# Kernel optimization log

Measured on AMD Instinct MI355X. Metric: run time of the kernel, lower is better.

Reference implementation:

```python
import jax, jax.numpy as jnp
import numpy as np

K = 5  # Chebyshev order


def laplacian(w):
    # normalized Laplacian: I - D^{-1/2} W D^{-1/2}
    d = jnp.sum(w, axis=1)
    d_re = 1.0 / jnp.sqrt(d + 1e-5)
    return jnp.eye(w.shape[0], dtype=w.dtype) - d_re[:, None] * w * d_re[None, :]


def cheb_terms(x, lap, k):
    # x: [B,N,C], lap: [N,N] -> [B,k,N,C]
    # Faithful to torch code: T0 = ones, then (x, lap@x) recurrence for k>2.
    t0 = jnp.ones_like(x)
    if k == 1:
        return t0[:, None]
    t1 = jnp.matmul(lap, x)
    if k == 2:
        return jnp.stack([t0, t1], axis=1)
    terms = [t0, x, t1]
    tkm1, tk = x, t1
    for _ in range(3, k):
        tkm1, tk = tk, 2.0 * jnp.matmul(lap, tk) - tkm1
        terms.append(tk)
    return jnp.stack(terms, axis=1)


def graph_conv(x, lap, w, k):
    # torch: cp.permute(0,2,3,1).flatten(2) @ w, i.e. flat index = c*k + t
    t = cheb_terms(x, lap, k)                       # [B,k,N,C]
    C = x.shape[-1]
    O = w.shape[-1]
    return jnp.einsum('bknc,cko->bno', t, w.reshape(C, k, O))


def setup_inputs() -> dict:
    key = jax.random.key(0)
    ks = jax.random.split(key, 9)
    B, N, Cin, H = 8192, 32, 60, 128
    return {
        'x': jax.random.normal(ks[0], (B, N, Cin), dtype=jnp.float32),
        'adj': jax.random.normal(ks[1], (N, N), dtype=jnp.float32) * 0.1,
        'adj_bias': jax.random.normal(ks[2], (1,), dtype=jnp.float32) * 0.1 + 0.2,
        'w1': jax.random.normal(ks[3], (K * Cin, H), dtype=jnp.float32) * 0.05,
        'b1': jax.random.normal(ks[4], (1, 1, H), dtype=jnp.float32) * 0.05,
        'w2': jax.random.normal(ks[5], (K * H, H), dtype=jnp.float32) * 0.05,
        'b2': jax.random.normal(ks[6], (1, 1, H), dtype=jnp.float32) * 0.05,
        'fc_w': jax.random.normal(ks[7], (2, N * H), dtype=jnp.float32) * 0.02,
        'fc_b': jax.random.normal(ks[8], (2,), dtype=jnp.float32) * 0.02,
    }


def reference(x, adj, adj_bias, w1, b1, w2, b2, fc_w, fc_b):
    # DGCNN.forward (eval mode: dropout = identity)
    a = jax.nn.relu(adj + adj_bias)
    lap = laplacian(a)
    h = graph_conv(x, lap, w1, K)
    h = jax.nn.relu(h + b1)      # B1ReLU
    h = graph_conv(h, lap, w2, K)
    h = jax.nn.relu(h + b2)
    h = h.reshape(h.shape[0], -1)  # [B, N*H]
    return h @ fc_w.T + fc_b
```

## Files before the change

### kernel.cpp

```cpp
#include <hip/hip_runtime.h>

typedef unsigned short u16;
typedef unsigned int u32;
typedef short bf16x8 __attribute__((ext_vector_type(8)));
typedef float f32x4 __attribute__((ext_vector_type(4)));

#define MFMA16(a, b, c) __builtin_amdgcn_mfma_f32_16x16x32_bf16((a), (b), (c), 0, 0, 0)

__device__ __forceinline__ u16 f2bf(float f) {
  u32 u = __builtin_bit_cast(u32, f);
  u += 0x7FFFu + ((u >> 16) & 1u);
  return (u16)(u >> 16);
}
__device__ __forceinline__ u32 pk2bf(float a, float b) {
#if __has_builtin(__builtin_amdgcn_cvt_pk_bf16_f32)
  auto v = __builtin_amdgcn_cvt_pk_bf16_f32(a, b);
  return __builtin_bit_cast(u32, v);
#else
  return (u32)f2bf(a) | ((u32)f2bf(b) << 16);
#endif
}

#define WS_MGF   0
#define WS_WT1F  8192
#define WS_WT2F  73728
#define WS_B1    204800
#define WS_B2    205312

__global__ void prep_kernel(const float* __restrict__ adj,
                            const float* __restrict__ adj_bias,
                            const float* __restrict__ w1,
                            const float* __restrict__ b1,
                            const float* __restrict__ w2,
                            const float* __restrict__ b2,
                            char* __restrict__ ws) {
  const int tid = threadIdx.x;
  if (blockIdx.x == 0) {
    __shared__ float sa[1024], Ls[1024], L2s[1024], L3s[1024], sdre[32];
    float bias = adj_bias[0];
    for (int i = tid; i < 1024; i += 256) sa[i] = fmaxf(adj[i] + bias, 0.0f);
    __syncthreads();
    if (tid < 32) {
      float s = 0.0f;
      for (int c = 0; c < 32; ++c) s += sa[tid * 32 + c];
      sdre[tid] = 1.0f / sqrtf(s + 1e-5f);
    }
    __syncthreads();
    for (int i = tid; i < 1024; i += 256) {
      int n = i >> 5, c = i & 31;
      Ls[i] = (n == c ? 1.0f : 0.0f) - sdre[n] * sa[i] * sdre[c];
    }
    __syncthreads();
    for (int i = tid; i < 1024; i += 256) {
      int r = i >> 5, c = i & 31;
      float s = 0.0f;
      for (int m = 0; m < 32; ++m) s += Ls[r * 32 + m] * Ls[m * 32 + c];
      L2s[i] = s;
    }
    __syncthreads();
    for (int i = tid; i < 1024; i += 256) {
      int r = i >> 5, c = i & 31;
      float s = 0.0f;
      for (int m = 0; m < 32; ++m) s += L2s[r * 32 + m] * Ls[m * 32 + c];
      L3s[i] = s;
    }
    __syncthreads();
    u16* MGf = (u16*)(ws + WS_MGF);
    for (int i = tid; i < 4096; i += 256) {
      int jt = i >> 9, lane = (i >> 3) & 63, j = i & 7;
      int col = jt * 16 + (lane & 15);
      int k = ((lane >> 4) << 3) + j;
      int kk = col >> 5, np = col & 31;
      float v;
      if (kk == 0)      v = (np == k) ? 1.0f : 0.0f;
      else if (kk == 1) v = Ls[np * 32 + k];
      else if (kk == 2) v = 2.0f * L2s[np * 32 + k] - (np == k ? 1.0f : 0.0f);
      else              v = 4.0f * L3s[np * 32 + k] - 3.0f * Ls[np * 32 + k];
      MGf[i] = f2bf(v);
    }
    float* B1 = (float*)(ws + WS_B1);
    float* B2 = (float*)(ws + WS_B2);
    if (tid < 128) {
      float s = b1[tid];
      for (int c = 0; c < 60; ++c) s += w1[(c * 5) * 128 + tid];
      B1[tid] = s;
    } else {
      int o = tid - 128;
      float s = b2[o];
      for (int c = 0; c < 128; ++c) s += w2[(c * 5) * 128 + o];
      B2[o] = s;
    }
  } else {
    u16* WT1F = (u16*)(ws + WS_WT1F);
    u16* WT2F = (u16*)(ws + WS_WT2F);
    int g = (blockIdx.x - 1) * 256 + tid;
    for (int i = g; i < 32768; i += 16 * 256) {
      int ot = i >> 12, ks = (i >> 9) & 7, lane = (i >> 3) & 63, j = i & 7;
      int o = ot * 16 + (lane & 15);
      int kc = ks * 32 + ((lane >> 4) << 3) + j;
      int k = kc >> 6, c = kc & 63;
      WT1F[i] = (c < 60) ? f2bf(w1[(c * 5 + k + 1) * 128 + o]) : (u16)0;
    }
    for (int i = g; i < 65536; i += 16 * 256) {
      int mt = i >> 13, h = (i >> 12) & 1, ks = (i >> 9) & 7;
      int lane = (i >> 3) & 63, j = i & 7;
      int kc = ((ks >> 1) << 7) + ((ks & 1) << 5) + (h << 6) + (((lane >> 4)) << 3) + j;
      int k = kc >> 7, c = kc & 127;
      int o = (mt << 4) + (lane & 15);
      WT2F[i] = f2bf(w2[(c * 5 + k + 1) * 128 + o]);
    }
  }
}

__global__ __launch_bounds__(256, 3) void dgcnn_kernel(
    const float* __restrict__ x,
    const char* __restrict__ ws,
    const float* __restrict__ fc_w,
    const float* __restrict__ fc_b,
    float* __restrict__ out) {
  __shared__ __align__(16) char arena[27136];
  __shared__ float red[8];
  u16* Xt = (u16*)arena;
  u16* Ht = (u16*)arena;
  u16* Y  = (u16*)(arena + 10240);

  const u16* MGf  = (const u16*)(ws + WS_MGF);
  const u16* WT1F = (const u16*)(ws + WS_WT1F);
  const u16* WT2F = (const u16*)(ws + WS_WT2F);
  const float* bias1 = (const float*)(ws + WS_B1);
  const float* bias2 = (const float*)(ws + WS_B2);

  const int tid = threadIdx.x;
  const int w = tid >> 6, lane = tid & 63;
  const int l15 = lane & 15, q = lane >> 4;
  const int b = blockIdx.x;
  const f32x4 z4 = {0.0f, 0.0f, 0.0f, 0.0f};

  bf16x8 mB0 = *(const bf16x8*)(MGf + ((2 * w + 0) * 64 + lane) * 8);
  bf16x8 mB1 = *(const bf16x8*)(MGf + ((2 * w + 1) * 64 + lane) * 8);
  bf16x8 wf1[16];
#pragma unroll
  for (int ot = 0; ot < 2; ++ot)
#pragma unroll
    for (int ks = 0; ks < 8; ++ks)
      wf1[ot * 8 + ks] = *(const bf16x8*)(WT1F + (((2 * w + ot) * 8 + ks) * 64 + lane) * 8);

  for (int i = tid; i < 160; i += 256) Xt[(60 + (i / 40)) * 40 + (i % 40)] = 0;
  const float* xb = x + (size_t)b * 1920;
  for (int i = tid; i < 1920; i += 256) {
    int n = i / 60, c = i - n * 60;
    Xt[c * 40 + n] = f2bf(xb[i]);
  }
  __syncthreads();

  {
    f32x4 acc[4][2];
#pragma unroll
    for (int mt = 0; mt < 4; ++mt) {
      bf16x8 aX = *(const bf16x8*)&Xt[(mt * 16 + l15) * 40 + q * 8];
      acc[mt][0] = MFMA16(aX, mB0, z4);
      acc[mt][1] = MFMA16(aX, mB1, z4);
    }
#pragma unroll
    for (int mt = 0; mt < 4; ++mt)
#pragma unroll
      for (int jt = 0; jt < 2; ++jt) {
        int np = jt * 16 + l15;
        uint2 vv;
        vv.x = pk2bf(acc[mt][jt][0], acc[mt][jt][1]);
        vv.y = pk2bf(acc[mt][jt][2], acc[mt][jt][3]);
        *(uint2*)&Y[np * 264 + w * 64 + mt * 16 + q * 4] = vv;
      }
  }
  __syncthreads();

  {
    f32x4 acc[2][2] = {{z4, z4}, {z4, z4}};
#pragma unroll
    for (int ks = 0; ks < 8; ++ks) {
      bf16x8 a0 = *(const bf16x8*)&Y[(l15) * 264 + ks * 32 + q * 8];
      bf16x8 a1 = *(const bf16x8*)&Y[(16 + l15) * 264 + ks * 32 + q * 8];
      acc[0][0] = MFMA16(a0, wf1[ks], acc[0][0]);
      acc[0][1] = MFMA16(a0, wf1[8 + ks], acc[0][1]);
      acc[1][0] = MFMA16(a1, wf1[ks], acc[1][0]);
      acc[1][1] = MFMA16(a1, wf1[8 + ks], acc[1][1]);
    }
#pragma unroll
    for (int ot = 0; ot < 2; ++ot) {
      int o = (2 * w + ot) * 16 + l15;
      float bv = bias1[o];
#pragma unroll
      for (int mt = 0; mt < 2; ++mt) {
        uint2 vv;
        vv.x = pk2bf(fmaxf(acc[mt][ot][0] + bv, 0.0f), fmaxf(acc[mt][ot][1] + bv, 0.0f));
        vv.y = pk2bf(fmaxf(acc[mt][ot][2] + bv, 0.0f), fmaxf(acc[mt][ot][3] + bv, 0.0f));
        *(uint2*)&Ht[o * 40 + mt * 16 + q * 4] = vv;
      }
    }
  }
  __syncthreads();

  f32x4 acc2[2][2] = {{z4, z4}, {z4, z4}};
#pragma unroll
  for (int h = 0; h < 2; ++h) {
    bf16x8 wf2[16];
#pragma unroll
    for (int ot = 0; ot < 2; ++ot)
#pragma unroll
      for (int ks = 0; ks < 8; ++ks)
        wf2[ot * 8 + ks] =
            *(const bf16x8*)(WT2F + ((((2 * w + ot) * 2 + h) * 8 + ks) * 64 + lane) * 8);

    {
      f32x4 acc[4][2];
#pragma unroll
      for (int mtl = 0; mtl < 4; ++mtl) {
        int mt = 4 * h + mtl;
        bf16x8 aH = *(const bf16x8*)&Ht[(mt * 16 + l15) * 40 + q * 8];
        acc[mtl][0] = MFMA16(aH, mB0, z4);
        acc[mtl][1] = MFMA16(aH, mB1, z4);
      }
#pragma unroll
      for (int mtl = 0; mtl < 4; ++mtl)
#pragma unroll
        for (int jt = 0; jt < 2; ++jt) {
          int np = jt * 16 + l15;
          uint2 vv;
          vv.x = pk2bf(acc[mtl][jt][0], acc[mtl][jt][1]);
          vv.y = pk2bf(acc[mtl][jt][2], acc[mtl][jt][3]);
          *(uint2*)&Y[np * 264 + w * 64 + mtl * 16 + q * 4] = vv;
        }
    }
    __syncthreads();
#pragma unroll
    for (int ks = 0; ks < 8; ++ks) {
      bf16x8 by0 = *(const bf16x8*)&Y[(l15) * 264 + ks * 32 + q * 8];
      bf16x8 by1 = *(const bf16x8*)&Y[(16 + l15) * 264 + ks * 32 + q * 8];
      acc2[0][0] = MFMA16(wf2[ks], by0, acc2[0][0]);
      acc2[0][1] = MFMA16(wf2[ks], by1, acc2[0][1]);
      acc2[1][0] = MFMA16(wf2[8 + ks], by0, acc2[1][0]);
      acc2[1][1] = MFMA16(wf2[8 + ks], by1, acc2[1][1]);
    }
    __syncthreads();
  }

  float p0 = 0.0f, p1 = 0.0f;
#pragma unroll
  for (int ot = 0; ot < 2; ++ot) {
    int ob = (2 * w + ot) * 16 + q * 4;
    float4 bv = *(const float4*)&bias2[ob];
#pragma unroll
    for (int nt = 0; nt < 2; ++nt) {
      int n = nt * 16 + l15;
      float h0 = fmaxf(acc2[ot][nt][0] + bv.x, 0.0f);
      float h1 = fmaxf(acc2[ot][nt][1] + bv.y, 0.0f);
      float h2 = fmaxf(acc2[ot][nt][2] + bv.z, 0.0f);
      float h3 = fmaxf(acc2[ot][nt][3] + bv.w, 0.0f);
      float4 w0 = *(const float4*)&fc_w[n * 128 + ob];
      float4 w1v = *(const float4*)&fc_w[4096 + n * 128 + ob];
      p0 = fmaf(h0, w0.x, fmaf(h1, w0.y, fmaf(h2, w0.z, fmaf(h3, w0.w, p0))));
      p1 = fmaf(h0, w1v.x, fmaf(h1, w1v.y, fmaf(h2, w1v.z, fmaf(h3, w1v.w, p1))));
    }
  }
#pragma unroll
  for (int off = 32; off >= 1; off >>= 1) {
    p0 += __shfl_xor(p0, off);
    p1 += __shfl_xor(p1, off);
  }
  if (lane == 0) {
    red[w * 2 + 0] = p0;
    red[w * 2 + 1] = p1;
  }
  __syncthreads();
  if (tid < 2) {
    out[b * 2 + tid] = red[tid] + red[2 + tid] + red[4 + tid] + red[6 + tid] + fc_b[tid];
  }
}

extern "C" void kernel_launch(void* const* d_in, const int* in_sizes, int n_in,
                              void* d_out, int out_size, void* d_ws, size_t ws_size,
                              hipStream_t stream) {
  const float* x        = (const float*)d_in[0];
  const float* adj      = (const float*)d_in[1];
  const float* adj_bias = (const float*)d_in[2];
  const float* w1       = (const float*)d_in[3];
  const float* b1       = (const float*)d_in[4];
  const float* w2       = (const float*)d_in[5];
  const float* b2       = (const float*)d_in[6];
  const float* fc_w     = (const float*)d_in[7];
  const float* fc_b     = (const float*)d_in[8];
  float* out = (float*)d_out;
  char* ws   = (char*)d_ws;

  prep_kernel<<<17, 256, 0, stream>>>(adj, adj_bias, w1, b1, w2, b2, ws);
  dgcnn_kernel<<<8192, 256, 0, stream>>>(x, ws, fc_w, fc_b, out);
}
```

Before: 206.5 us.

## Process two batch samples per block to reuse weight fragments

Each block now handles two graph samples with duplicated LDS buffers and accumulators, halving the grid to 4096 blocks. Weight fragments for both layers (and the Laplacian fragments) are loaded once and applied to both samples, cutting the global weight traffic and fixed per-block overhead per sample. The first-layer weights are now loaded inside the k-loop instead of held in registers. The H tile stride is also shrunk from 40 to 36. The cost is about double the LDS per block (~52KB) and more accumulator registers, which may lower occupancy.

```diff
diff --git a/kernel.cpp b/kernel.cpp
--- a/kernel.cpp
+++ b/kernel.cpp
@@ -118,11 +118,14 @@
     const float* __restrict__ fc_w,
     const float* __restrict__ fc_b,
     float* __restrict__ out) {
-  __shared__ __align__(16) char arena[27136];
-  __shared__ float red[8];
-  u16* Xt = (u16*)arena;
-  u16* Ht = (u16*)arena;
-  u16* Y  = (u16*)(arena + 10240);
+  __shared__ __align__(16) char arena[52224];
+  __shared__ float red[16];
+  u16* XtA = (u16*)arena;
+  u16* XtB = (u16*)(arena + 5120);
+  u16* HtA = (u16*)arena;
+  u16* HtB = (u16*)(arena + 9216);
+  u16* YA  = (u16*)(arena + 18432);
+  u16* YB  = (u16*)(arena + 35328);
 
   const u16* MGf  = (const u16*)(ws + WS_MGF);
   const u16* WT1F = (const u16*)(ws + WS_WT1F);
@@ -133,57 +136,73 @@
   const int tid = threadIdx.x;
   const int w = tid >> 6, lane = tid & 63;
   const int l15 = lane & 15, q = lane >> 4;
-  const int b = blockIdx.x;
+  const int b0 = blockIdx.x * 2;
   const f32x4 z4 = {0.0f, 0.0f, 0.0f, 0.0f};
 
   bf16x8 mB0 = *(const bf16x8*)(MGf + ((2 * w + 0) * 64 + lane) * 8);
   bf16x8 mB1 = *(const bf16x8*)(MGf + ((2 * w + 1) * 64 + lane) * 8);
-  bf16x8 wf1[16];
-#pragma unroll
-  for (int ot = 0; ot < 2; ++ot)
-#pragma unroll
-    for (int ks = 0; ks < 8; ++ks)
-      wf1[ot * 8 + ks] = *(const bf16x8*)(WT1F + (((2 * w + ot) * 8 + ks) * 64 + lane) * 8);
-
-  for (int i = tid; i < 160; i += 256) Xt[(60 + (i / 40)) * 40 + (i % 40)] = 0;
-  const float* xb = x + (size_t)b * 1920;
+
+  for (int i = tid; i < 160; i += 256) {
+    int r = 60 + i / 40, c = i % 40;
+    XtA[r * 40 + c] = 0;
+    XtB[r * 40 + c] = 0;
+  }
+  const float* xb = x + (size_t)b0 * 1920;
   for (int i = tid; i < 1920; i += 256) {
     int n = i / 60, c = i - n * 60;
-    Xt[c * 40 + n] = f2bf(xb[i]);
+    XtA[c * 40 + n] = f2bf(xb[i]);
+    XtB[c * 40 + n] = f2bf(xb[1920 + i]);
   }
   __syncthreads();
 
   {
-    f32x4 acc[4][2];
+    f32x4 accA[4][2], accB[4][2];
 #pragma unroll
     for (int mt = 0; mt < 4; ++mt) {
-      bf16x8 aX = *(const bf16x8*)&Xt[(mt * 16 + l15) * 40 + q * 8];
-      acc[mt][0] = MFMA16(aX, mB0, z4);
-      acc[mt][1] = MFMA16(aX, mB1, z4);
+      bf16x8 aXA = *(const bf16x8*)&XtA[(mt * 16 + l15) * 40 + q * 8];
+      bf16x8 aXB = *(const bf16x8*)&XtB[(mt * 16 + l15) * 40 + q * 8];
+      accA[mt][0] = MFMA16(aXA, mB0, z4);
+      accA[mt][1] = MFMA16(aXA, mB1, z4);
+      accB[mt][0] = MFMA16(aXB, mB0, z4);
+      accB[mt][1] = MFMA16(aXB, mB1, z4);
     }
 #pragma unroll
     for (int mt = 0; mt < 4; ++mt)
 #pragma unroll
       for (int jt = 0; jt < 2; ++jt) {
         int np = jt * 16 + l15;
-        uint2 vv;
-        vv.x = pk2bf(acc[mt][jt][0], acc[mt][jt][1]);
-        vv.y = pk2bf(acc[mt][jt][2], acc[mt][jt][3]);
-        *(uint2*)&Y[np * 264 + w * 64 + mt * 16 + q * 4] = vv;
+        int off = np * 264 + w * 64 + mt * 16 + q * 4;
+        uint2 vA, vB;
+        vA.x = pk2bf(accA[mt][jt][0], accA[mt][jt][1]);
+        vA.y = pk2bf(accA[mt][jt][2], accA[mt][jt][3]);
+        vB.x = pk2bf(accB[mt][jt][0], accB[mt][jt][1]);
+        vB.y = pk2bf(accB[mt][jt][2], accB[mt][jt][3]);
+        *(uint2*)&YA[off] = vA;
+        *(uint2*)&YB[off] = vB;
       }
   }
   __syncthreads();
 
   {
-    f32x4 acc[2][2] = {{z4, z4}, {z4, z4}};
+    f32x4 accA[2][2] = {{z4, z4}, {z4, z4}};
+    f32x4 accB[2][2] = {{z4, z4}, {z4, z4}};
 #pragma unroll
     for (int ks = 0; ks < 8; ++ks) {
-      bf16x8 a0 = *(const bf16x8*)&Y[(l15) * 264 + ks * 32 + q * 8];
-      bf16x8 a1 = *(const bf16x8*)&Y[(16 + l15) * 264 + ks * 32 + q * 8];
-      acc[0][0] = MFMA16(a0, wf1[ks], acc[0][0]);
-      acc[0][1] = MFMA16(a0, wf1[8 + ks], acc[0][1]);
-      acc[1][0] = MFMA16(a1, wf1[ks], acc[1][0]);
-      acc[1][1] = MFMA16(a1, wf1[8 + ks], acc[1][1]);
+      bf16x8 wfa = *(const bf16x8*)(WT1F + (((2 * w + 0) * 8 + ks) * 64 + lane) * 8);
+      bf16x8 wfb = *(const bf16x8*)(WT1F + (((2 * w + 1) * 8 + ks) * 64 + lane) * 8);
+      int offY = ks * 32 + q * 8;
+      bf16x8 a0A = *(const bf16x8*)&YA[(l15) * 264 + offY];
+      bf16x8 a1A = *(const bf16x8*)&YA[(16 + l15) * 264 + offY];
+      bf16x8 a0B = *(const bf16x8*)&YB[(l15) * 264 + offY];
+      bf16x8 a1B = *(const bf16x8*)&YB[(16 + l15) * 264 + offY];
+      accA[0][0] = MFMA16(a0A, wfa, accA[0][0]);
+      accA[0][1] = MFMA16(a0A, wfb, accA[0][1]);
+      accA[1][0] = MFMA16(a1A, wfa, accA[1][0]);
+      accA[1][1] = MFMA16(a1A, wfb, accA[1][1]);
+      accB[0][0] = MFMA16(a0B, wfa, accB[0][0]);
+      accB[0][1] = MFMA16(a0B, wfb, accB[0][1]);
+      accB[1][0] = MFMA16(a1B, wfa, accB[1][0]);
+      accB[1][1] = MFMA16(a1B, wfb, accB[1][1]);
     }
 #pragma unroll
     for (int ot = 0; ot < 2; ++ot) {
@@ -191,16 +210,21 @@
       float bv = bias1[o];
 #pragma unroll
       for (int mt = 0; mt < 2; ++mt) {
-        uint2 vv;
-        vv.x = pk2bf(fmaxf(acc[mt][ot][0] + bv, 0.0f), fmaxf(acc[mt][ot][1] + bv, 0.0f));
-        vv.y = pk2bf(fmaxf(acc[mt][ot][2] + bv, 0.0f), fmaxf(acc[mt][ot][3] + bv, 0.0f));
-        *(uint2*)&Ht[o * 40 + mt * 16 + q * 4] = vv;
+        int off = o * 36 + mt * 16 + q * 4;
+        uint2 vA, vB;
+        vA.x = pk2bf(fmaxf(accA[mt][ot][0] + bv, 0.0f), fmaxf(accA[mt][ot][1] + bv, 0.0f));
+        vA.y = pk2bf(fmaxf(accA[mt][ot][2] + bv, 0.0f), fmaxf(accA[mt][ot][3] + bv, 0.0f));
+        vB.x = pk2bf(fmaxf(accB[mt][ot][0] + bv, 0.0f), fmaxf(accB[mt][ot][1] + bv, 0.0f));
+        vB.y = pk2bf(fmaxf(accB[mt][ot][2] + bv, 0.0f), fmaxf(accB[mt][ot][3] + bv, 0.0f));
+        *(uint2*)&HtA[off] = vA;
+        *(uint2*)&HtB[off] = vB;
       }
     }
   }
   __syncthreads();
 
-  f32x4 acc2[2][2] = {{z4, z4}, {z4, z4}};
+  f32x4 acc2A[2][2] = {{z4, z4}, {z4, z4}};
+  f32x4 acc2B[2][2] = {{z4, z4}, {z4, z4}};
 #pragma unroll
   for (int h = 0; h < 2; ++h) {
     bf16x8 wf2[16];
@@ -212,39 +236,53 @@
             *(const bf16x8*)(WT2F + ((((2 * w + ot) * 2 + h) * 8 + ks) * 64 + lane) * 8);
 
     {
-      f32x4 acc[4][2];
+      f32x4 accA[4][2], accB[4][2];
 #pragma unroll
       for (int mtl = 0; mtl < 4; ++mtl) {
-        int mt = 4 * h + mtl;
-        bf16x8 aH = *(const bf16x8*)&Ht[(mt * 16 + l15) * 40 + q * 8];
-        acc[mtl][0] = MFMA16(aH, mB0, z4);
-        acc[mtl][1] = MFMA16(aH, mB1, z4);
+        int r = ((4 * h + mtl) * 16 + l15) * 36 + q * 8;
+        bf16x8 aHA = *(const bf16x8*)&HtA[r];
+        bf16x8 aHB = *(const bf16x8*)&HtB[r];
+        accA[mtl][0] = MFMA16(aHA, mB0, z4);
+        accA[mtl][1] = MFMA16(aHA, mB1, z4);
+        accB[mtl][0] = MFMA16(aHB, mB0, z4);
+        accB[mtl][1] = MFMA16(aHB, mB1, z4);
       }
 #pragma unroll
       for (int mtl = 0; mtl < 4; ++mtl)
 #pragma unroll
         for (int jt = 0; jt < 2; ++jt) {
           int np = jt * 16 + l15;
-          uint2 vv;
-          vv.x = pk2bf(acc[mtl][jt][0], acc[mtl][jt][1]);
-          vv.y = pk2bf(acc[mtl][jt][2], acc[mtl][jt][3]);
-          *(uint2*)&Y[np * 264 + w * 64 + mtl * 16 + q * 4] = vv;
+          int off = np * 264 + w * 64 + mtl * 16 + q * 4;
+          uint2 vA, vB;
+          vA.x = pk2bf(accA[mtl][jt][0], accA[mtl][jt][1]);
+          vA.y = pk2bf(accA[mtl][jt][2], accA[mtl][jt][3]);
+          vB.x = pk2bf(accB[mtl][jt][0], accB[mtl][jt][1]);
+          vB.y = pk2bf(accB[mtl][jt][2], accB[mtl][jt][3]);
+          *(uint2*)&YA[off] = vA;
+          *(uint2*)&YB[off] = vB;
         }
     }
     __syncthreads();
 #pragma unroll
     for (int ks = 0; ks < 8; ++ks) {
-      bf16x8 by0 = *(const bf16x8*)&Y[(l15) * 264 + ks * 32 + q * 8];
-      bf16x8 by1 = *(const bf16x8*)&Y[(16 + l15) * 264 + ks * 32 + q * 8];
-      acc2[0][0] = MFMA16(wf2[ks], by0, acc2[0][0]);
-      acc2[0][1] = MFMA16(wf2[ks], by1, acc2[0][1]);
-      acc2[1][0] = MFMA16(wf2[8 + ks], by0, acc2[1][0]);
-      acc2[1][1] = MFMA16(wf2[8 + ks], by1, acc2[1][1]);
-    }
-    __syncthreads();
-  }
-
-  float p0 = 0.0f, p1 = 0.0f;
+      int offY = ks * 32 + q * 8;
+      bf16x8 by0A = *(const bf16x8*)&YA[(l15) * 264 + offY];
+      bf16x8 by1A = *(const bf16x8*)&YA[(16 + l15) * 264 + offY];
+      bf16x8 by0B = *(const bf16x8*)&YB[(l15) * 264 + offY];
+      bf16x8 by1B = *(const bf16x8*)&YB[(16 + l15) * 264 + offY];
+      acc2A[0][0] = MFMA16(wf2[ks], by0A, acc2A[0][0]);
+      acc2A[0][1] = MFMA16(wf2[ks], by1A, acc2A[0][1]);
+      acc2A[1][0] = MFMA16(wf2[8 + ks], by0A, acc2A[1][0]);
+      acc2A[1][1] = MFMA16(wf2[8 + ks], by1A, acc2A[1][1]);
+      acc2B[0][0] = MFMA16(wf2[ks], by0B, acc2B[0][0]);
+      acc2B[0][1] = MFMA16(wf2[ks], by1B, acc2B[0][1]);
+      acc2B[1][0] = MFMA16(wf2[8 + ks], by0B, acc2B[1][0]);
+      acc2B[1][1] = MFMA16(wf2[8 + ks], by1B, acc2B[1][1]);
+    }
+    __syncthreads();
+  }
+
+  float p0A = 0.0f, p1A = 0.0f, p0B = 0.0f, p1B = 0.0f;
 #pragma unroll
   for (int ot = 0; ot < 2; ++ot) {
     int ob = (2 * w + ot) * 16 + q * 4;
@@ -252,28 +290,39 @@
 #pragma unroll
     for (int nt = 0; nt < 2; ++nt) {
       int n = nt * 16 + l15;
-      float h0 = fmaxf(acc2[ot][nt][0] + bv.x, 0.0f);
-      float h1 = fmaxf(acc2[ot][nt][1] + bv.y, 0.0f);
-      float h2 = fmaxf(acc2[ot][nt][2] + bv.z, 0.0f);
-      float h3 = fmaxf(acc2[ot][nt][3] + bv.w, 0.0f);
       float4 w0 = *(const float4*)&fc_w[n * 128 + ob];
       float4 w1v = *(const float4*)&fc_w[4096 + n * 128 + ob];
-      p0 = fmaf(h0, w0.x, fmaf(h1, w0.y, fmaf(h2, w0.z, fmaf(h3, w0.w, p0))));
-      p1 = fmaf(h0, w1v.x, fmaf(h1, w1v.y, fmaf(h2, w1v.z, fmaf(h3, w1v.w, p1))));
+      float hA0 = fmaxf(acc2A[ot][nt][0] + bv.x, 0.0f);
+      float hA1 = fmaxf(acc2A[ot][nt][1] + bv.y, 0.0f);
+      float hA2 = fmaxf(acc2A[ot][nt][2] + bv.z, 0.0f);
+      float hA3 = fmaxf(acc2A[ot][nt][3] + bv.w, 0.0f);
+      float hB0 = fmaxf(acc2B[ot][nt][0] + bv.x, 0.0f);
+      float hB1 = fmaxf(acc2B[ot][nt][1] + bv.y, 0.0f);
+      float hB2 = fmaxf(acc2B[ot][nt][2] + bv.z, 0.0f);
+      float hB3 = fmaxf(acc2B[ot][nt][3] + bv.w, 0.0f);
+      p0A = fmaf(hA0, w0.x, fmaf(hA1, w0.y, fmaf(hA2, w0.z, fmaf(hA3, w0.w, p0A))));
+      p1A = fmaf(hA0, w1v.x, fmaf(hA1, w1v.y, fmaf(hA2, w1v.z, fmaf(hA3, w1v.w, p1A))));
+      p0B = fmaf(hB0, w0.x, fmaf(hB1, w0.y, fmaf(hB2, w0.z, fmaf(hB3, w0.w, p0B))));
+      p1B = fmaf(hB0, w1v.x, fmaf(hB1, w1v.y, fmaf(hB2, w1v.z, fmaf(hB3, w1v.w, p1B))));
     }
   }
 #pragma unroll
   for (int off = 32; off >= 1; off >>= 1) {
-    p0 += __shfl_xor(p0, off);
-    p1 += __shfl_xor(p1, off);
+    p0A += __shfl_xor(p0A, off);
+    p1A += __shfl_xor(p1A, off);
+    p0B += __shfl_xor(p0B, off);
+    p1B += __shfl_xor(p1B, off);
   }
   if (lane == 0) {
-    red[w * 2 + 0] = p0;
-    red[w * 2 + 1] = p1;
+    red[w * 4 + 0] = p0A;
+    red[w * 4 + 1] = p1A;
+    red[w * 4 + 2] = p0B;
+    red[w * 4 + 3] = p1B;
   }
   __syncthreads();
-  if (tid < 2) {
-    out[b * 2 + tid] = red[tid] + red[2 + tid] + red[4 + tid] + red[6 + tid] + fc_b[tid];
+  if (tid < 4) {
+    float s = red[tid] + red[4 + tid] + red[8 + tid] + red[12 + tid] + fc_b[tid & 1];
+    out[(b0 + (tid >> 1)) * 2 + (tid & 1)] = s;
   }
 }
 
@@ -293,5 +342,5 @@
   char* ws   = (char*)d_ws;
 
   prep_kernel<<<17, 256, 0, stream>>>(adj, adj_bias, w1, b1, w2, b2, ws);
-  dgcnn_kernel<<<8192, 256, 0, stream>>>(x, ws, fc_w, fc_b, out);
-}
+  dgcnn_kernel<<<4096, 256, 0, stream>>>(x, ws, fc_w, fc_b, out);
+}
```

Measured after the change: 203.2 us. No clear change (-1.6%).
